# Kernel optimization log

Measured on AMD Instinct MI355X. Metric: run time of the kernel, lower is better.

Reference implementation:

```python
import jax, jax.numpy as jnp
import numpy as np

NUM = 256
T = 0.05
MAXITER = 5


def _constants():
    P = jnp.eye(NUM, dtype=jnp.float32)                  # [num, num]
    Pd = jnp.diff(P, axis=0) / T                          # [num-1, num]
    Pdd = jnp.diff(Pd, axis=0) / T                        # [num-2, num]
    A_eq = P[0:1]                                         # [1, num]
    A_control = jnp.vstack([P, -P, Pd, -Pd, Pdd, -Pdd])   # [6*num-6, num]
    # rho = rho_projection = 1, A_projection = I
    cost = jnp.eye(NUM, dtype=jnp.float32) + A_control.T @ A_control
    cost_mat = jnp.vstack([
        jnp.hstack([cost, A_eq.T]),
        jnp.hstack([A_eq, jnp.zeros((1, 1), dtype=jnp.float32)]),
    ])                                                    # [num+1, num+1]
    return A_eq, A_control, cost_mat


def setup_inputs() -> dict:
    key = jax.random.key(0)
    ks = jax.random.split(key, 8)
    B, IND, H = 4096, 260, 1024
    NC = 6 * NUM - 6
    OUT = NUM + NC
    return {
        "inp": jax.random.normal(ks[0], (B, IND), jnp.float32),
        "steer_init": 0.1 * jax.random.normal(ks[1], (B, 1), jnp.float32),
        "steer_samples": 0.5 * jax.random.normal(ks[2], (B, NUM), jnp.float32),
        "steer_max": jnp.float32(1.0),
        "steer_min": jnp.float32(-1.0),
        "steerdot_max": jnp.float32(2.0),
        "steerdot_min": jnp.float32(-2.0),
        "steerddot_max": jnp.float32(4.0),
        "steerddot_min": jnp.float32(-4.0),
        "median_": jnp.zeros((IND,), jnp.float32),
        "iqr_": jnp.ones((IND,), jnp.float32),
        "W1": 0.02 * jax.random.normal(ks[3], (IND, H), jnp.float32),
        "b1": jnp.zeros((H,), jnp.float32),
        "W2": 0.02 * jax.random.normal(ks[4], (H, OUT), jnp.float32),
        "b2": jnp.zeros((OUT,), jnp.float32),
    }


def reference(inp, steer_init, steer_samples, steer_max, steer_min,
              steerdot_max, steerdot_min, steerddot_max, steerddot_min,
              median_, iqr_, W1, b1, W2, b2):
    A_eq, A_control, cost_mat = _constants()
    B = inp.shape[0]
    NC = A_control.shape[0]
    n1, n2 = NUM - 1, NUM - 2

    # Note: original computes (inp-median)/iqr then overwrites with inp.
    inp_norm = inp
    h = jax.nn.relu(inp_norm @ W1 + b1)
    neural_out = h @ W2 + b2                              # [B, num + nc]
    lamda = neural_out[:, :NUM]
    s = jnp.maximum(0.0, neural_out[:, NUM:NUM + NC])

    b_eq = steer_init * jnp.ones((B, 1), jnp.float32)     # [B, 1]
    ones_n = jnp.ones((B, NUM), jnp.float32)
    ones_n1 = jnp.ones((B, n1), jnp.float32)
    ones_n2 = jnp.ones((B, n2), jnp.float32)
    b_control = jnp.hstack([
        steer_max * ones_n, -steer_min * ones_n,
        steerdot_max * ones_n1, -steerdot_min * ones_n1,
        steerddot_max * ones_n2, -steerddot_min * ones_n2,
    ])                                                    # [B, nc]

    def step(carry, _):
        lamda, s = carry
        b_aug = b_control - s
        # rho = rho_projection = 1, A_projection = I
        lincost = -lamda - steer_samples - b_aug @ A_control   # [B, num]
        rhs = jnp.hstack([-lincost, b_eq])                     # [B, num+1]
        sol = jnp.linalg.solve(cost_mat, rhs.T).T
        steer_proj = sol[:, :NUM]
        As = steer_proj @ A_control.T                          # [B, nc]
        s_new = jnp.maximum(0.0, -As + b_control)
        res_vec = As - b_control + s_new
        res_norm = jnp.linalg.norm(res_vec, axis=1)
        lamda_new = lamda - res_vec @ A_control
        fp = (jnp.linalg.norm(s - s_new, axis=1)
              + jnp.linalg.norm(lamda - lamda_new, axis=1))
        return (lamda_new, s_new), (steer_proj, res_norm, fp)

    (_, _), (projs, prim_stack, fp_stack) = jax.lax.scan(
        step, (lamda, s), None, length=MAXITER)
    steer_projected = projs[-1]
    acc_primal = jnp.sum(prim_stack, axis=0) / MAXITER
    acc_fixed = jnp.sum(fp_stack, axis=0) / MAXITER
    return steer_projected, prim_stack, fp_stack, acc_primal, acc_fixed
```

## Files before the change

### kernel.cpp

```cpp
#include <hip/hip_runtime.h>
#include <cstddef>


#define NUMV 256
#define QP_ITERS 5
#define NO_LD 1792
#define LSCALE 2048.0f
#define INV_LSCALE (1.0f / 2048.0f)

typedef _Float16 f16x4 __attribute__((ext_vector_type(4)));
typedef _Float16 f16x8 __attribute__((ext_vector_type(8)));
typedef float f32x4 __attribute__((ext_vector_type(4)));

struct FacT {
  double invd[256];
  double l1[257];
  double l2[258];
  double z[256];
  float  zcf[256];
};

constexpr double csqrt_(double x) {
  double g = (x > 1.0) ? x : 1.0;
  for (int i = 0; i < 64; ++i) g = 0.5 * (g + x / g);
  return g;
}

constexpr FacT make_fac() {
  FacT f{};
  const double T = 0.05, a = 1.0 / (T * T), b2 = a * a;
  double c0[256] = {}, c1[255] = {}, c2[254] = {};
  double dd[256] = {}, l1[256] = {}, l2[256] = {};
  for (int j = 0; j < 256; j++) {
    double cd1 = (j == 0 || j == 255) ? 1.0 : 2.0;
    double cd2 = (j == 0 || j == 255) ? 1.0 : ((j == 1 || j == 254) ? 5.0 : 6.0);
    c0[j] = 3.0 + 2.0 * a * cd1 + 2.0 * b2 * cd2;
  }
  for (int j = 0; j < 255; j++) c1[j] = -2.0 * a + 2.0 * b2 * ((j == 0 || j == 254) ? -2.0 : -4.0);
  for (int j = 0; j < 254; j++) c2[j] = 2.0 * b2;
  dd[0] = csqrt_(c0[0]); l1[0] = 0.0; l2[0] = 0.0;
  l1[1] = c1[0] / dd[0]; l2[1] = 0.0;
  dd[1] = csqrt_(c0[1] - l1[1] * l1[1]);
  for (int j = 2; j < 256; j++) {
    l2[j] = c2[j - 2] / dd[j - 2];
    l1[j] = (c1[j - 1] - l2[j] * l1[j - 1]) / dd[j - 1];
    dd[j] = csqrt_(c0[j] - l1[j] * l1[j] - l2[j] * l2[j]);
  }
  for (int j = 0; j < 256; j++) f.invd[j] = 1.0 / dd[j];
  for (int j = 0; j < 256; j++) f.l1[j] = l1[j];
  f.l1[256] = 0.0;
  for (int j = 0; j < 256; j++) f.l2[j] = l2[j];
  f.l2[256] = 0.0; f.l2[257] = 0.0;
  double w[256] = {}, zz[256] = {};
  w[0] = 1.0 / dd[0];
  w[1] = (-l1[1] * w[0]) / dd[1];
  for (int j = 2; j < 256; j++) w[j] = (-l1[j] * w[j - 1] - l2[j] * w[j - 2]) / dd[j];
  zz[255] = w[255] / dd[255];
  zz[254] = (w[254] - l1[255] * zz[255]) / dd[254];
  for (int j = 253; j >= 0; j--)
    zz[j] = (w[j] - l1[j + 1] * zz[j + 1] - l2[j + 2] * zz[j + 2]) / dd[j];
  for (int j = 0; j < 256; j++) f.z[j] = zz[j];
  for (int j = 0; j < 256; j++) f.zcf[j] = (float)(zz[j] / zz[0]);
  return f;
}

constexpr FacT FAC_HOST = make_fac();
__constant__ FacT FAC = FAC_HOST;

struct UQ { float u[64][256]; };

constexpr UQ make_uq(int cbase) {
  UQ q{};
  const double T = 0.05, a = 1.0 / (T * T), b2 = a * a;
  double c0a[256] = {}, c1a[255] = {}, c2a[254] = {};
  double dd[256] = {}, l1[256] = {}, l2[256] = {};
  for (int j = 0; j < 256; j++) {
    double cd1 = (j == 0 || j == 255) ? 1.0 : 2.0;
    double cd2 = (j == 0 || j == 255) ? 1.0 : ((j == 1 || j == 254) ? 5.0 : 6.0);
    c0a[j] = 3.0 + 2.0 * a * cd1 + 2.0 * b2 * cd2;
  }
  for (int j = 0; j < 255; j++) c1a[j] = -2.0 * a + 2.0 * b2 * ((j == 0 || j == 254) ? -2.0 : -4.0);
  for (int j = 0; j < 254; j++) c2a[j] = 2.0 * b2;
  dd[0] = csqrt_(c0a[0]); l1[0] = 0.0; l2[0] = 0.0;
  l1[1] = c1a[0] / dd[0]; l2[1] = 0.0;
  dd[1] = csqrt_(c0a[1] - l1[1] * l1[1]);
  for (int j = 2; j < 256; j++) {
    l2[j] = c2a[j - 2] / dd[j - 2];
    l1[j] = (c1a[j - 1] - l2[j] * l1[j - 1]) / dd[j - 1];
    dd[j] = csqrt_(c0a[j] - l1[j] * l1[j] - l2[j] * l2[j]);
  }
  for (int c = cbase; c < cbase + 64; ++c) {
    double w1 = 0.0, w2 = 0.0;
    for (int j = c; j < 256; ++j) {
      const double rhs = (j == c) ? 1.0 : 0.0;
      const double wj = (rhs - l1[j] * w1 - l2[j] * w2) / dd[j];
      q.u[c - cbase][j] = (float)wj;
      w2 = w1; w1 = wj;
    }
  }
  return q;
}

constexpr UQ UQ0_H = make_uq(0);
constexpr UQ UQ1_H = make_uq(64);
constexpr UQ UQ2_H = make_uq(128);
constexpr UQ UQ3_H = make_uq(192);
__constant__ UQ UFQ0 = UQ0_H;
__constant__ UQ UFQ1 = UQ1_H;
__constant__ UQ UFQ2 = UQ2_H;
__constant__ UQ UFQ3 = UQ3_H;

__device__ __forceinline__ const float* uq_row(int c) {
  if (c < 64)  return UFQ0.u[c];
  if (c < 128) return UFQ1.u[c - 64];
  if (c < 192) return UFQ2.u[c - 128];
  return UFQ3.u[c - 192];
}

__device__ __forceinline__ void split8(const float* __restrict__ w, f16x8& h, f16x8& l) {
#pragma unroll
  for (int e = 0; e < 8; e++) {
    const float x = w[e];
    const _Float16 hh = (_Float16)x;
    h[e] = hh;
    l[e] = (_Float16)((x - (float)hh) * LSCALE);
  }
}

__device__ void gemm_g_body(
    _Float16* __restrict__ Gh, _Float16* __restrict__ Gl, float* __restrict__ zc,
    int gx, int gy, int lane)
{
  const int lr = lane & 15, lg = lane >> 4;
  const int m0 = gx * 16, n0 = gy * 32;
  if (gx == 0 && gy == 0) {
    for (int t = lane; t < 256; t += 64) zc[t] = FAC.zcf[t];
  }
  f32x4 accH[2], accL[2];
#pragma unroll
  for (int nf = 0; nf < 2; nf++) { accH[nf] = (f32x4)0.0f; accL[nf] = (f32x4)0.0f; }
  const float* arow = uq_row(m0 + lr);
  const float* brow0 = uq_row(n0 + lr);
  const float* brow1 = uq_row(n0 + 16 + lr);
#pragma unroll 2
  for (int k0 = 0; k0 < 256; k0 += 32) {
    f16x8 ah, al;
    split8(arow + k0 + lg * 8, ah, al);
#pragma unroll
    for (int nf = 0; nf < 2; nf++) {
      f16x8 bh, bl;
      split8((nf ? brow1 : brow0) + k0 + lg * 8, bh, bl);
      accH[nf] = __builtin_amdgcn_mfma_f32_16x16x32_f16(ah, bh, accH[nf], 0, 0, 0);
      accL[nf] = __builtin_amdgcn_mfma_f32_16x16x32_f16(ah, bl, accL[nf], 0, 0, 0);
      accL[nf] = __builtin_amdgcn_mfma_f32_16x16x32_f16(al, bh, accL[nf], 0, 0, 0);
    }
  }
  const int row0 = m0 + lg * 4;
#pragma unroll
  for (int nf = 0; nf < 2; nf++) {
    const int col = n0 + nf * 16 + lr;
    const double zcd = FAC.z[col] / FAC.z[0];
#pragma unroll
    for (int r = 0; r < 4; r++) {
      const int row = row0 + r;
      const float g = accH[nf][r] + accL[nf][r] * INV_LSCALE
                    - (float)(FAC.z[row] * zcd);
      const _Float16 gh = (_Float16)g;
      Gh[(size_t)row * 256 + col] = gh;
      Gl[(size_t)row * 256 + col] = (_Float16)((g - (float)gh) * LSCALE);
    }
  }
}

__device__ void transpose_body(
    const float* __restrict__ in, _Float16* __restrict__ out,
    int K, int N, int KP, int bx, int by, int tid)
{
  __shared__ float t[32][33];
  const int bk = bx * 32, bn = by * 32;
  const int x = tid & 31, y = tid >> 5;
  for (int yy = y; yy < 32; yy += 8) {
    const int k = bk + yy, n = bn + x;
    t[yy][x] = (k < K && n < N) ? in[(size_t)k * N + n] : 0.f;
  }
  __syncthreads();
  for (int yy = y; yy < 32; yy += 8) {
    const int n = bn + yy, k = bk + x;
    if (n < N && k < KP) out[(size_t)n * KP + k] = (_Float16)t[x][yy];
  }
}

#define PREP_G   128
#define PREP_T1  288
#define PREP_T2  1792
#define PREP_CV  256
__global__ __launch_bounds__(256) void prep(
    _Float16* __restrict__ Gh, _Float16* __restrict__ Gl, float* __restrict__ zc,
    const float* __restrict__ W1, _Float16* __restrict__ W1T,
    const float* __restrict__ W2, _Float16* __restrict__ W2T,
    const float* __restrict__ inp, _Float16* __restrict__ hA,
    int IND, int OUTN)
{
  const int bid = blockIdx.x;
  const int tid = threadIdx.x;
  if (bid < PREP_G) {
    if (tid < 64) gemm_g_body(Gh, Gl, zc, bid & 15, bid >> 4, tid);
  } else if (bid < PREP_G + PREP_T1) {
    const int i = bid - PREP_G;
    transpose_body(W1, W1T, IND, 1024, 288, i % 9, i / 9, tid);
  } else if (bid < PREP_G + PREP_T1 + PREP_T2) {
    const int i = bid - PREP_G - PREP_T1;
    transpose_body(W2, W2T, 1024, OUTN, 1024, i & 31, i >> 5, tid);
  } else {
    const int r0 = (bid - PREP_G - PREP_T1 - PREP_T2) * 16;
    for (int idx = tid; idx < 16 * 288; idx += 256) {
      const int r = r0 + idx / 288, c = idx % 288;
      hA[(size_t)r * 288 + c] =
          (c < IND) ? (_Float16)inp[(size_t)r * IND + c] : (_Float16)0.f;
    }
  }
}

__global__ __launch_bounds__(256) void mfma_gemm32(
    const _Float16* __restrict__ A, const _Float16* __restrict__ Bt,
    const float* __restrict__ bias, _Float16* __restrict__ C,
    int KP, int ldc)
{
  __shared__ _Float16 At[128][32];
  __shared__ _Float16 Bs[128][32];
  const int tid = threadIdx.x;
  const int lane = tid & 63, wid = tid >> 6;
  const int wr = wid >> 1, wc = wid & 1;
  const int lrow = lane & 15, lb = lane >> 4;
  const int m0 = blockIdx.x * 128, n0 = blockIdx.y * 128;
  const int rl4 = lane >> 2;
  const int kswz = 8 * ((lane & 3) ^ (rl4 & 3));

  f32x4 acc[4][4];
#pragma unroll
  for (int i = 0; i < 4; i++)
#pragma unroll
    for (int j = 0; j < 4; j++) acc[i][j] = (f32x4)0.0f;

  const int nsteps = KP >> 5;
  for (int t = 0; t < nsteps; ++t) {
    const int k0 = t * 32;
#pragma unroll
    for (int c = 0; c < 2; ++c) {
      const int ci = wid * 2 + c;
      const _Float16* asrc = &A[(size_t)(m0 + ci * 16 + rl4) * KP + k0 + kswz];
      const _Float16* bsrc = &Bt[(size_t)(n0 + ci * 16 + rl4) * KP + k0 + kswz];
      __builtin_amdgcn_global_load_lds(
          (const __attribute__((address_space(1))) void*)asrc,
          (__attribute__((address_space(3))) void*)(&At[ci * 16][0]), 16, 0, 0);
      __builtin_amdgcn_global_load_lds(
          (const __attribute__((address_space(1))) void*)bsrc,
          (__attribute__((address_space(3))) void*)(&Bs[ci * 16][0]), 16, 0, 0);
    }
    __syncthreads();
    f16x8 af[4], bf[4];
#pragma unroll
    for (int i = 0; i < 4; i++) {
      const int r = wr * 64 + i * 16 + lrow;
      af[i] = *reinterpret_cast<const f16x8*>(&At[r][(lb * 8) ^ ((r & 3) << 3)]);
    }
#pragma unroll
    for (int j = 0; j < 4; j++) {
      const int r = wc * 64 + j * 16 + lrow;
      bf[j] = *reinterpret_cast<const f16x8*>(&Bs[r][(lb * 8) ^ ((r & 3) << 3)]);
    }
#pragma unroll
    for (int i = 0; i < 4; i++)
#pragma unroll
      for (int j = 0; j < 4; j++)
        acc[i][j] = __builtin_amdgcn_mfma_f32_16x16x32_f16(af[i], bf[j], acc[i][j], 0, 0, 0);
    __syncthreads();
  }
#pragma unroll
  for (int i = 0; i < 4; i++) {
#pragma unroll
    for (int j = 0; j < 4; j++) {
      const int gcol = n0 + wc * 64 + j * 16 + lrow;
      const float bv = bias[gcol];
#pragma unroll
      for (int r = 0; r < 4; r++) {
        const int grow = m0 + wr * 64 + i * 16 + lb * 4 + r;
        const float v = fmaxf(acc[i][j][r] + bv, 0.f);
        C[(size_t)grow * ldc + gcol] = (_Float16)v;
      }
    }
  }
}

__global__ __launch_bounds__(256) void mfma_gemm64(
    const _Float16* __restrict__ A, const _Float16* __restrict__ Bt,
    const float* __restrict__ bias, float* __restrict__ C,
    int M, int Nv, int K, int lda, int ldk, int ldc)
{
  __shared__ _Float16 At[128][64];
  __shared__ _Float16 Bs[128][64];
  const int tid = threadIdx.x;
  const int lane = tid & 63, wid = tid >> 6;
  const int wr = wid >> 1, wc = wid & 1;
  const int lrow = lane & 15, lb = lane >> 4;
  const int m0 = blockIdx.x * 128, n0 = blockIdx.y * 128;

  const int srow8 = lane >> 3;
  const int kswz = 8 * ((lane & 7) ^ srow8);

  f32x4 acc[4][4];
#pragma unroll
  for (int i = 0; i < 4; i++)
#pragma unroll
    for (int j = 0; j < 4; j++) acc[i][j] = (f32x4)0.0f;

  const int nsteps = K >> 6;
  for (int t = 0; t < nsteps; ++t) {
    const int k0 = t * 64;
#pragma unroll
    for (int c = 0; c < 4; ++c) {
      const int ci = wid * 4 + c;
      const int row = ci * 8 + srow8;
      const _Float16* asrc = &A[(size_t)(m0 + row) * lda + k0 + kswz];
      const _Float16* bsrc = &Bt[(size_t)(n0 + row) * ldk + k0 + kswz];
      __builtin_amdgcn_global_load_lds(
          (const __attribute__((address_space(1))) void*)asrc,
          (__attribute__((address_space(3))) void*)(&At[ci * 8][0]), 16, 0, 0);
      __builtin_amdgcn_global_load_lds(
          (const __attribute__((address_space(1))) void*)bsrc,
          (__attribute__((address_space(3))) void*)(&Bs[ci * 8][0]), 16, 0, 0);
    }
    __syncthreads();
#pragma unroll
    for (int h = 0; h < 2; h++) {
      f16x8 af[4], bf[4];
#pragma unroll
      for (int i = 0; i < 4; i++) {
        const int r = wr * 64 + i * 16 + lrow;
        af[i] = *reinterpret_cast<const f16x8*>(
            &At[r][(h * 32 + lb * 8) ^ ((r & 7) << 3)]);
      }
#pragma unroll
      for (int j = 0; j < 4; j++) {
        const int r = wc * 64 + j * 16 + lrow;
        bf[j] = *reinterpret_cast<const f16x8*>(
            &Bs[r][(h * 32 + lb * 8) ^ ((r & 7) << 3)]);
      }
#pragma unroll
      for (int i = 0; i < 4; i++)
#pragma unroll
        for (int j = 0; j < 4; j++)
          acc[i][j] = __builtin_amdgcn_mfma_f32_16x16x32_f16(af[i], bf[j], acc[i][j], 0, 0, 0);
    }
    __syncthreads();
  }
#pragma unroll
  for (int i = 0; i < 4; i++) {
#pragma unroll
    for (int j = 0; j < 4; j++) {
      const int gcol = n0 + wc * 64 + j * 16 + lrow;
      if (gcol < Nv) {
        const float bv = bias[gcol];
#pragma unroll
        for (int r = 0; r < 4; r++) {
          const int grow = m0 + wr * 64 + i * 16 + lb * 4 + r;
          C[(size_t)grow * ldc + gcol] = acc[i][j][r] + bv;
        }
      }
    }
  }
}

__global__ __launch_bounds__(1024) void qp_solve5(
    const _Float16* __restrict__ Gh, const _Float16* __restrict__ Gl,
    const float* __restrict__ beq, const float* __restrict__ zc,
    const float* __restrict__ NO, const float* __restrict__ ss,
    const float* __restrict__ p_smax, const float* __restrict__ p_smin,
    const float* __restrict__ p_sdmax, const float* __restrict__ p_sdmin,
    const float* __restrict__ p_sddmax, const float* __restrict__ p_sddmin,
    float* __restrict__ out, int B)
{
  __shared__ float xsA[16][264], xsB[16][264];
  __shared__ _Float16 vhs[16][264], vls[16][264];
  __shared__ float zcs[256], beqs[16];
  __shared__ float red[16][4][3];
  const int tid = threadIdx.x;
  const int wave = tid >> 6, lane = tid & 63;
  const int lr = lane & 15, lg = lane >> 4;
  const int m0 = blockIdx.x * 16;
  const int n0 = wave * 16;
  const int j = tid & 255, half = tid >> 8;

  const float smax = *p_smax, smin = *p_smin;
  const float sdmax = *p_sdmax, sdmin = *p_sdmin;
  const float sddmax = *p_sddmax, sddmin = *p_sddmin;
  const float K0 = smax + smin, K1 = sdmax + sdmin, K2 = sddmax + sddmin;
  const float invT = 20.f, invT2 = 400.f;
  const bool h1 = j < 255, h2 = j < 254;

  f16x8 gh_r[8];
#pragma unroll
  for (int kk = 0; kk < 8; kk++) {
    const size_t bidx = (size_t)(n0 + lr) * 256 + kk * 32 + lg * 8;
    gh_r[kk] = *reinterpret_cast<const f16x8*>(&Gh[bidx]);
  }

  float lamr[4], ssv[4];
#pragma unroll
  for (int rr = 0; rr < 4; rr++) {
    const int rl = half * 4 + rr;
    const int gr = m0 + rl;
    const float* no = NO + (size_t)gr * NO_LD;
    ssv[rr] = ss[(size_t)gr * NUMV + j];
    lamr[rr] = no[j];
    const float D0 = K0 - fmaxf(0.f, no[256 + j]) + fmaxf(0.f, no[512 + j]);
    const float D1j = h1 ? (K1 - fmaxf(0.f, no[768 + j]) + fmaxf(0.f, no[1023 + j])) : 0.f;
    const float D1m = (j >= 1) ? (K1 - fmaxf(0.f, no[768 + j - 1]) + fmaxf(0.f, no[1023 + j - 1])) : 0.f;
    const float D2j = h2 ? (K2 - fmaxf(0.f, no[1278 + j]) + fmaxf(0.f, no[1532 + j])) : 0.f;
    const float D2m1 = (j >= 1 && h1) ? (K2 - fmaxf(0.f, no[1278 + j - 1]) + fmaxf(0.f, no[1532 + j - 1])) : 0.f;
    const float D2m2 = (j >= 2) ? (K2 - fmaxf(0.f, no[1278 + j - 2]) + fmaxf(0.f, no[1532 + j - 2])) : 0.f;
    const float vn = lamr[rr] + ssv[rr]
                   + D0 + (D1m - D1j) * invT + (D2m2 - 2.f * D2m1 + D2j) * invT2;
    const _Float16 vh16 = (_Float16)vn;
    vhs[rl][j] = vh16;
    vls[rl][j] = (_Float16)((vn - (float)vh16) * LSCALE);
  }
  if (tid < 256) zcs[tid] = zc[tid];
  if (tid < 16) {
    beqs[tid] = beq[m0 + tid];
    xsA[tid][0] = 0.f; xsA[tid][1] = 0.f; xsA[tid][258] = 0.f; xsA[tid][259] = 0.f;
    xsB[tid][0] = 0.f; xsB[tid][1] = 0.f; xsB[tid][258] = 0.f; xsB[tid][259] = 0.f;
  }
  float accP = 0.f, accF = 0.f;

  const size_t primOff = (size_t)B * NUMV;
  const size_t fpOff = primOff + (size_t)QP_ITERS * B;
  const size_t accPOff = fpOff + (size_t)QP_ITERS * B;
  const size_t accFOff = accPOff + (size_t)B;

  float (*xc)[264] = xsA;
  float (*xp)[264] = xsB;

  __syncthreads();

  for (int it = 0; it < QP_ITERS; ++it) {
    f32x4 accH = (f32x4)0.0f, accL = (f32x4)0.0f;
#pragma unroll
    for (int kk = 0; kk < 8; kk++) {
      const f16x8 ah = *reinterpret_cast<const f16x8*>(&vhs[lr][kk * 32 + lg * 8]);
      const f16x8 al = *reinterpret_cast<const f16x8*>(&vls[lr][kk * 32 + lg * 8]);
      const f16x8 bl = *reinterpret_cast<const f16x8*>(
          &Gl[(size_t)(n0 + lr) * 256 + kk * 32 + lg * 8]);
      accH = __builtin_amdgcn_mfma_f32_16x16x32_f16(ah, gh_r[kk], accH, 0, 0, 0);
      accL = __builtin_amdgcn_mfma_f32_16x16x32_f16(ah, bl, accL, 0, 0, 0);
      accL = __builtin_amdgcn_mfma_f32_16x16x32_f16(al, gh_r[kk], accL, 0, 0, 0);
    }
    {
      const int r0l = lg * 4;
      const int col = n0 + lr;
      const float zv = zcs[col];
#pragma unroll
      for (int r = 0; r < 4; r++)
        xc[r0l + r][col + 2] = accH[r] + accL[r] * INV_LSCALE + beqs[r0l + r] * zv;
    }
    __syncthreads();

#pragma unroll
    for (int rr = 0; rr < 4; rr++) {
      const int rl = half * 4 + rr;
      const int gr = m0 + rl;
      const float xm2 = xc[rl][j];
      const float xm1 = xc[rl][j + 1];
      const float x0  = xc[rl][j + 2];
      const float x1  = xc[rl][j + 3];
      const float x2  = xc[rl][j + 4];

      const float vj = (x1 - x0) * invT;
      const float aj = (x2 - 2.f * x1 + x0) * invT2;
      const float vm1 = (x0 - xm1) * invT;
      const float am1 = (x1 - 2.f * x0 + xm1) * invT2;
      const float am2 = (x0 - 2.f * xm1 + xm2) * invT2;

      const float rv0a = fmaxf(0.f, x0 - smax), rv0b = fmaxf(0.f, smin - x0);
      const float E0 = rv0a - rv0b;
      float rv1a = 0.f, rv1b = 0.f, rv2a = 0.f, rv2b = 0.f, E1 = 0.f, E2 = 0.f;
      if (h1) { rv1a = fmaxf(0.f, vj - sdmax); rv1b = fmaxf(0.f, sdmin - vj); E1 = rv1a - rv1b; }
      if (h2) { rv2a = fmaxf(0.f, aj - sddmax); rv2b = fmaxf(0.f, sddmin - aj); E2 = rv2a - rv2b; }
      float res2 = rv0a * rv0a + rv0b * rv0b + rv1a * rv1a + rv1b * rv1b
                 + rv2a * rv2a + rv2b * rv2b;

      const float E1m = (j >= 1) ? (fmaxf(0.f, vm1 - sdmax) - fmaxf(0.f, sdmin - vm1)) : 0.f;
      const float E2m1 = (j >= 1 && h1) ? (fmaxf(0.f, am1 - sddmax) - fmaxf(0.f, sddmin - am1)) : 0.f;
      const float E2m2 = (j >= 2) ? (fmaxf(0.f, am2 - sddmax) - fmaxf(0.f, sddmin - am2)) : 0.f;

      const float dl = E0 + (E1m - E1) * invT + (E2m2 - 2.f * E2m1 + E2) * invT2;
      const float lnew = lamr[rr] - dl;
      const float fpl2 = dl * dl;
      lamr[rr] = lnew;

      const float sn0a = fmaxf(0.f, smax - x0), sn0b = fmaxf(0.f, x0 - smin);
      float sn1a = 0.f, sn1b = 0.f, sn2a = 0.f, sn2b = 0.f;
      if (h1) { sn1a = fmaxf(0.f, sdmax - vj); sn1b = fmaxf(0.f, vj - sdmin); }
      if (h2) { sn2a = fmaxf(0.f, sddmax - aj); sn2b = fmaxf(0.f, aj - sddmin); }

      float sp0a, sp0b, sp1a = 0.f, sp1b = 0.f, sp2a = 0.f, sp2b = 0.f;
      if (it == 0) {
        const float* no = NO + (size_t)gr * NO_LD;
        sp0a = fmaxf(0.f, no[256 + j]); sp0b = fmaxf(0.f, no[512 + j]);
        if (h1) { sp1a = fmaxf(0.f, no[768 + j]); sp1b = fmaxf(0.f, no[1023 + j]); }
        if (h2) { sp2a = fmaxf(0.f, no[1278 + j]); sp2b = fmaxf(0.f, no[1532 + j]); }
      } else {
        const float p0 = xp[rl][j + 2], p1 = xp[rl][j + 3], p2 = xp[rl][j + 4];
        const float vp = (p1 - p0) * invT;
        const float ap = (p2 - 2.f * p1 + p0) * invT2;
        sp0a = fmaxf(0.f, smax - p0); sp0b = fmaxf(0.f, p0 - smin);
        if (h1) { sp1a = fmaxf(0.f, sdmax - vp); sp1b = fmaxf(0.f, vp - sdmin); }
        if (h2) { sp2a = fmaxf(0.f, sddmax - ap); sp2b = fmaxf(0.f, ap - sddmin); }
      }
      const float d0a = sp0a - sn0a, d0b = sp0b - sn0b;
      const float d1a = sp1a - sn1a, d1b = sp1b - sn1b;
      const float d2a = sp2a - sn2a, d2b = sp2b - sn2b;
      float fps2 = d0a * d0a + d0b * d0b + d1a * d1a + d1b * d1b
                 + d2a * d2a + d2b * d2b;

      const float D0 = fminf(smax, x0) + fmaxf(smin, x0);
      const float D1 = h1 ? (fminf(sdmax, vj) + fmaxf(sdmin, vj)) : 0.f;
      const float D2 = h2 ? (fminf(sddmax, aj) + fmaxf(sddmin, aj)) : 0.f;
      const float D1m = (j >= 1) ? (fminf(sdmax, vm1) + fmaxf(sdmin, vm1)) : 0.f;
      const float D2m1 = (j >= 1 && h1) ? (fminf(sddmax, am1) + fmaxf(sddmin, am1)) : 0.f;
      const float D2m2 = (j >= 2) ? (fminf(sddmax, am2) + fmaxf(sddmin, am2)) : 0.f;

      if (it < QP_ITERS - 1) {
        const float vn = lnew + ssv[rr]
                       + D0 + (D1m - D1) * invT + (D2m2 - 2.f * D2m1 + D2) * invT2;
        const _Float16 vh16 = (_Float16)vn;
        vhs[rl][j] = vh16;
        vls[rl][j] = (_Float16)((vn - (float)vh16) * LSCALE);
      } else {
        out[(size_t)gr * NUMV + j] = x0;
      }

      float a = res2, b = fps2, c = fpl2;
      for (int o = 32; o > 0; o >>= 1) {
        a += __shfl_down(a, o);
        b += __shfl_down(b, o);
        c += __shfl_down(c, o);
      }
      if (lane == 0) { red[wave][rr][0] = a; red[wave][rr][1] = b; red[wave][rr][2] = c; }
    }
    __syncthreads();

    if (tid < 16) {
      const int rl = tid, hf = rl >> 2, rr = rl & 3;
      const int w0 = hf * 4;
      const float r2 = red[w0][rr][0] + red[w0 + 1][rr][0] + red[w0 + 2][rr][0] + red[w0 + 3][rr][0];
      const float s2 = red[w0][rr][1] + red[w0 + 1][rr][1] + red[w0 + 2][rr][1] + red[w0 + 3][rr][1];
      const float l2 = red[w0][rr][2] + red[w0 + 1][rr][2] + red[w0 + 2][rr][2] + red[w0 + 3][rr][2];
      const float pr = sqrtf(r2);
      const float fp = sqrtf(s2) + sqrtf(l2);
      out[primOff + (size_t)it * B + m0 + rl] = pr;
      out[fpOff + (size_t)it * B + m0 + rl] = fp;
      accP += pr; accF += fp;
    }
    float (*t)[264] = xc; xc = xp; xp = t;
  }
  if (tid < 16) {
    out[accPOff + m0 + tid] = accP * (1.f / QP_ITERS);
    out[accFOff + m0 + tid] = accF * (1.f / QP_ITERS);
  }
}

extern "C" void kernel_launch(void* const* d_in, const int* in_sizes, int n_in,
                              void* d_out, int out_size, void* d_ws, size_t ws_size,
                              hipStream_t stream)
{
  const float* inp = (const float*)d_in[0];
  const float* sinit = (const float*)d_in[1];
  const float* ssamp = (const float*)d_in[2];
  const float* p_smax = (const float*)d_in[3];
  const float* p_smin = (const float*)d_in[4];
  const float* p_sdmax = (const float*)d_in[5];
  const float* p_sdmin = (const float*)d_in[6];
  const float* p_sddmax = (const float*)d_in[7];
  const float* p_sddmin = (const float*)d_in[8];
  const float* W1 = (const float*)d_in[11];
  const float* b1 = (const float*)d_in[12];
  const float* W2 = (const float*)d_in[13];
  const float* b2 = (const float*)d_in[14];
  float* out = (float*)d_out;

  const int B = in_sizes[1];
  const int IND = in_sizes[9];
  const int H = in_sizes[12];
  const int OUTN = in_sizes[14];
  const int KP1 = 288;

  char* ws = (char*)d_ws;
  float* NO = (float*)ws;
  char* p = ws + (size_t)B * NO_LD * 4;
  _Float16* hH = (_Float16*)p;
  char* q = p + (size_t)B * H * 2;
  _Float16* W2T = (_Float16*)q;
  char* q2 = q + (size_t)OUTN * H * 2;
  _Float16* W1T = (_Float16*)q2;
  _Float16* hA = (_Float16*)(q2 + (size_t)H * KP1 * 2);
  char* r4 = ws + 46137344;
  _Float16* Gh = (_Float16*)r4;
  _Float16* Gl = (_Float16*)(r4 + 131072);
  float* zc = (float*)(r4 + 262144);

  prep<<<PREP_G + PREP_T1 + PREP_T2 + PREP_CV, 256, 0, stream>>>(
      Gh, Gl, zc, W1, W1T, W2, W2T, inp, hA, IND, OUTN);
  {
    dim3 g(B / 128, H / 128);
    mfma_gemm32<<<g, 256, 0, stream>>>(hA, W1T, b1, hH, KP1, H);
  }
  {
    dim3 g(B / 128, (OUTN + 127) / 128);
    mfma_gemm64<<<g, 256, 0, stream>>>(hH, W2T, b2, NO, B, OUTN, H, H, H, NO_LD);
  }
  qp_solve5<<<B / 16, 1024, 0, stream>>>(Gh, Gl, sinit, zc, NO, ssamp,
                                         p_smax, p_smin, p_sdmax, p_sdmin,
                                         p_sddmax, p_sddmin, out, B);
}
```

Baseline: 119.2 us.

## Overlap W2 transpose and G factorization with first GEMM in one launch

Splits the prep kernel so only the W1 transpose and input conversion run before the first GEMM. The first GEMM, the cost-matrix factorization and the W2 transpose are then merged into one kernel with block-index dispatch. This lets the independent prep work fill the GPU alongside GEMM1 instead of sitting on the critical path before it. Launch count stays the same, but heterogeneous blocks in one grid may balance unevenly, and GEMM1 blocks share the CUs with transpose blocks.

```diff
diff --git a/kernel.cpp b/kernel.cpp
--- a/kernel.cpp
+++ b/kernel.cpp
@@ -190,49 +190,17 @@
   }
 }
 
-#define PREP_G   128
-#define PREP_T1  288
-#define PREP_T2  1792
-#define PREP_CV  256
-__global__ __launch_bounds__(256) void prep(
-    _Float16* __restrict__ Gh, _Float16* __restrict__ Gl, float* __restrict__ zc,
-    const float* __restrict__ W1, _Float16* __restrict__ W1T,
-    const float* __restrict__ W2, _Float16* __restrict__ W2T,
-    const float* __restrict__ inp, _Float16* __restrict__ hA,
-    int IND, int OUTN)
-{
-  const int bid = blockIdx.x;
-  const int tid = threadIdx.x;
-  if (bid < PREP_G) {
-    if (tid < 64) gemm_g_body(Gh, Gl, zc, bid & 15, bid >> 4, tid);
-  } else if (bid < PREP_G + PREP_T1) {
-    const int i = bid - PREP_G;
-    transpose_body(W1, W1T, IND, 1024, 288, i % 9, i / 9, tid);
-  } else if (bid < PREP_G + PREP_T1 + PREP_T2) {
-    const int i = bid - PREP_G - PREP_T1;
-    transpose_body(W2, W2T, 1024, OUTN, 1024, i & 31, i >> 5, tid);
-  } else {
-    const int r0 = (bid - PREP_G - PREP_T1 - PREP_T2) * 16;
-    for (int idx = tid; idx < 16 * 288; idx += 256) {
-      const int r = r0 + idx / 288, c = idx % 288;
-      hA[(size_t)r * 288 + c] =
-          (c < IND) ? (_Float16)inp[(size_t)r * IND + c] : (_Float16)0.f;
-    }
-  }
-}
-
-__global__ __launch_bounds__(256) void mfma_gemm32(
+__device__ void gemm1_body(
     const _Float16* __restrict__ A, const _Float16* __restrict__ Bt,
     const float* __restrict__ bias, _Float16* __restrict__ C,
-    int KP, int ldc)
+    int KP, int ldc, int bx, int by, int tid)
 {
   __shared__ _Float16 At[128][32];
   __shared__ _Float16 Bs[128][32];
-  const int tid = threadIdx.x;
   const int lane = tid & 63, wid = tid >> 6;
   const int wr = wid >> 1, wc = wid & 1;
   const int lrow = lane & 15, lb = lane >> 4;
-  const int m0 = blockIdx.x * 128, n0 = blockIdx.y * 128;
+  const int m0 = bx * 128, n0 = by * 128;
   const int rl4 = lane >> 2;
   const int kswz = 8 * ((lane & 3) ^ (rl4 & 3));
 
@@ -289,6 +257,46 @@
         C[(size_t)grow * ldc + gcol] = (_Float16)v;
       }
     }
+  }
+}
+
+#define P1_T1 288
+#define P1_CV 256
+__global__ __launch_bounds__(256) void prep1(
+    const float* __restrict__ W1, _Float16* __restrict__ W1T,
+    const float* __restrict__ inp, _Float16* __restrict__ hA, int IND)
+{
+  const int bid = blockIdx.x, tid = threadIdx.x;
+  if (bid < P1_T1) {
+    transpose_body(W1, W1T, IND, 1024, 288, bid % 9, bid / 9, tid);
+  } else {
+    const int r0 = (bid - P1_T1) * 16;
+    for (int idx = tid; idx < 16 * 288; idx += 256) {
+      const int r = r0 + idx / 288, c = idx % 288;
+      hA[(size_t)r * 288 + c] =
+          (c < IND) ? (_Float16)inp[(size_t)r * IND + c] : (_Float16)0.f;
+    }
+  }
+}
+
+#define G1_BLKS 256
+#define GG_BLKS 128
+#define T2_BLKS 1792
+__global__ __launch_bounds__(256) void gemm1_fused(
+    const _Float16* __restrict__ hA, const _Float16* __restrict__ W1T,
+    const float* __restrict__ b1, _Float16* __restrict__ hH,
+    _Float16* __restrict__ Gh, _Float16* __restrict__ Gl, float* __restrict__ zc,
+    const float* __restrict__ W2, _Float16* __restrict__ W2T, int OUTN)
+{
+  const int bid = blockIdx.x, tid = threadIdx.x;
+  if (bid < G1_BLKS) {
+    gemm1_body(hA, W1T, b1, hH, 288, 1024, bid & 31, bid >> 5, tid);
+  } else if (bid < G1_BLKS + GG_BLKS) {
+    const int i = bid - G1_BLKS;
+    if (tid < 64) gemm_g_body(Gh, Gl, zc, i & 15, i >> 4, tid);
+  } else {
+    const int i = bid - G1_BLKS - GG_BLKS;
+    transpose_body(W2, W2T, 1024, OUTN, 1024, i & 31, i >> 5, tid);
   }
 }
 
@@ -609,12 +617,9 @@
   _Float16* Gl = (_Float16*)(r4 + 131072);
   float* zc = (float*)(r4 + 262144);
 
-  prep<<<PREP_G + PREP_T1 + PREP_T2 + PREP_CV, 256, 0, stream>>>(
-      Gh, Gl, zc, W1, W1T, W2, W2T, inp, hA, IND, OUTN);
-  {
-    dim3 g(B / 128, H / 128);
-    mfma_gemm32<<<g, 256, 0, stream>>>(hA, W1T, b1, hH, KP1, H);
-  }
+  prep1<<<P1_T1 + P1_CV, 256, 0, stream>>>(W1, W1T, inp, hA, IND);
+  gemm1_fused<<<G1_BLKS + GG_BLKS + T2_BLKS, 256, 0, stream>>>(
+      hA, W1T, b1, hH, Gh, Gl, zc, W2, W2T, OUTN);
   {
     dim3 g(B / 128, (OUTN + 127) / 128);
     mfma_gemm64<<<g, 256, 0, stream>>>(hH, W2T, b2, NO, B, OUTN, H, H, H, NO_LD);
```

Measured after the change: 118.2 us. Within noise of the previous version (-0.9%).
